# Optimization experiments

Measured on AMD Instinct MI355X. Metric: run time of the kernel, lower is better.

The kernel has to match this reference:

```python
import jax, jax.numpy as jnp
import numpy as np

N, D, H, K = 131072, 512, 128, 3
NPOS, NNEG = 8192, 8192
KM_ITERS = 4
PROTO_SHIFT = 0.15
PROTO_LOGIT_SCALE = 0.2
TEMP = 2.5


def _sq_cdist(x, c):
    # squared euclidean distance, matches torch.cdist(...).pow(2)
    d = jnp.sum(x * x, -1, keepdims=True) + jnp.sum(c * c, -1)[None, :] - 2.0 * (x @ c.T)
    return jnp.maximum(d, 0.0)


def _kmeans(x, k, iters):
    # torch.linspace(0, n-1, steps=k).long() init, fixed iteration count
    n = x.shape[0]
    idx = jnp.linspace(0.0, n - 1, k).astype(jnp.int32)
    centers = x[idx]
    for _ in range(iters):
        assign = jnp.argmin(_sq_cdist(x, centers), axis=1)
        sums = jax.ops.segment_sum(x, assign, num_segments=k)
        counts = jax.ops.segment_sum(jnp.ones((n,), x.dtype), assign, num_segments=k)[:, None]
        # empty cluster keeps old center (mask.any() branch in torch)
        centers = jnp.where(counts > 0, sums / jnp.maximum(counts, 1.0), centers)
    return centers


def setup_inputs() -> dict:
    key = jax.random.key(0)
    ks = jax.random.split(key, 10)
    s = 1.0 / np.sqrt(D).astype(np.float32)
    return {
        "z_cls": jax.random.normal(ks[0], (N, D), jnp.float32),
        "z_proto": jax.random.normal(ks[1], (N, D), jnp.float32),
        "pos_ctx": jax.random.normal(ks[2], (D,), jnp.float32),
        "neg_ctx": jax.random.normal(ks[3], (D,), jnp.float32),
        "W1": jax.random.normal(ks[4], (H, D), jnp.float32) * s,
        "b1": jnp.zeros((H,), jnp.float32),
        "W2": jax.random.normal(ks[5], (1, H), jnp.float32) * (1.0 / np.sqrt(H).astype(np.float32)),
        "b2": jnp.zeros((1,), jnp.float32),
        "Wp": jax.random.normal(ks[6], (D, D), jnp.float32) * s,
        "bp": jnp.zeros((D,), jnp.float32),
        "Wn": jax.random.normal(ks[7], (D, D), jnp.float32) * s,
        "bn": jnp.zeros((D,), jnp.float32),
        "pos_idx": jax.random.randint(ks[8], (NPOS,), 0, N),
        "neg_idx": jax.random.randint(ks[9], (NNEG,), 0, N),
    }


def reference(z_cls, z_proto, pos_ctx, neg_ctx, W1, b1, W2, b2, Wp, bp, Wn, bn, pos_idx, neg_idx):
    # _build_prototypes (pos_idx/neg_idx nonempty path)
    pos_proto = _kmeans(z_proto[pos_idx], K, KM_ITERS)          # [K, D]
    neg_proto = jnp.mean(z_proto[neg_idx], axis=0)              # [D]
    # _calibrate (ema not initialized -> no EMA blend)
    pos_proto = pos_proto + PROTO_SHIFT * (pos_ctx @ Wp.T + bp)[None, :]
    neg_proto = neg_proto + PROTO_SHIFT * (neg_ctx @ Wn.T + bn)
    # distances
    d_pos_all = _sq_cdist(z_proto, pos_proto)                   # [N, K]
    d_pos = jnp.min(d_pos_all, axis=1)
    pos_assign = jnp.argmin(d_pos_all, axis=1)
    d_neg = jnp.mean((z_proto - neg_proto[None, :]) ** 2, axis=1)
    proto_logit = (d_neg - d_pos) / np.sqrt(D).astype(np.float32)
    # cls head (eval mode: dropout is identity)
    h = jax.nn.relu(z_cls @ W1.T + b1)
    cls_logit = (h @ W2.T + b2)[:, 0]
    logits = (cls_logit + PROTO_LOGIT_SCALE * proto_logit) / TEMP
    prob = jax.nn.sigmoid(logits)
    return (logits, prob, PROTO_LOGIT_SCALE * proto_logit, pos_assign, d_pos_all, pos_proto, neg_proto)
```

## Files before the change

kernel.cpp:

```cpp
#include <hip/hip_runtime.h>
#include <hip/hip_bf16.h>

#define NPTS 131072
#define DIM  512
#define HID  128
#define KCL  3
#define NPOSI 8192
#define NNEGI 8192

typedef __attribute__((ext_vector_type(8))) short bf16x8;
typedef __attribute__((ext_vector_type(4))) float f32x4;

enum {
  WS_SHIFT_POS = 0,
  WS_SHIFT_NEG = 512,
  WS_NEGSUM    = 1024,
  WS_NEGPART   = 1536,
  WS_SUMS      = 67072,
  WS_W1BF      = 73228,
};
#define SUMS_STRIDE 1539

__device__ __forceinline__ short f2bf(float x) {
  __hip_bfloat16 h = __float2bfloat16(x);
  return *reinterpret_cast<short*>(&h);
}

__global__ __launch_bounds__(256) void k_prep(const float* __restrict__ W1,
                                              const float* __restrict__ Wp, const float* __restrict__ bp,
                                              const float* __restrict__ Wn, const float* __restrict__ bn,
                                              const float* __restrict__ pos_ctx, const float* __restrict__ neg_ctx,
                                              const float* __restrict__ zp, const int* __restrict__ neg_idx,
                                              float* __restrict__ ws) {
  int bid = blockIdx.x, t = threadIdx.x;
  if (bid < 256) {
    int i = bid * 256 + t;
    __hip_bfloat16* dst = (__hip_bfloat16*)(ws + WS_W1BF);
    dst[i] = __float2bfloat16(W1[i]);
  } else if (bid < 288) {
    int b = bid - 256;
    int mat = b >> 4;
    const float* W    = mat ? Wn : Wp;
    const float* bias = mat ? bn : bp;
    const float* ctx  = mat ? neg_ctx : pos_ctx;
    float* outp = ws + (mat ? WS_SHIFT_NEG : WS_SHIFT_POS);
    int row = (b & 15) * 32 + (t >> 3);
    int sub = t & 7;
    const float* wr = W + row * DIM + sub * 64;
    const float* cr = ctx + sub * 64;
    float s = 0.f;
#pragma unroll
    for (int j = 0; j < 64; j += 4) {
      float4 w4 = *(const float4*)(wr + j);
      float4 c4 = *(const float4*)(cr + j);
      s += w4.x * c4.x + w4.y * c4.y + w4.z * c4.z + w4.w * c4.w;
    }
    s += __shfl_xor(s, 1);
    s += __shfl_xor(s, 2);
    s += __shfl_xor(s, 4);
    if (sub == 0) outp[row] = 0.15f * (s + bias[row]);
  } else if (bid < 416) {
    int j = bid - 288;
    int c0 = t * 2;
    float a0 = 0.f, a1 = 0.f;
    int j0 = j * 64;
    for (int jj = 0; jj < 64; ++jj) {
      int row = neg_idx[j0 + jj];
      float2 v = *(const float2*)(zp + (size_t)row * DIM + c0);
      a0 += v.x; a1 += v.y;
    }
    ws[WS_NEGPART + j * DIM + c0]     = a0;
    ws[WS_NEGPART + j * DIM + c0 + 1] = a1;
  } else {
    for (int idx = t; idx < 4 * SUMS_STRIDE; idx += 256) ws[WS_SUMS + idx] = 0.f;
  }
}

template <int IT>
__global__ __launch_bounds__(256) void k_km(const float* __restrict__ zp,
                                            const int* __restrict__ pos_idx,
                                            float* __restrict__ ws) {
  int bid = blockIdx.x, t = threadIdx.x;
  if (IT == 0 && bid == 128) {
    int c0 = t * 2;
    float a0 = 0.f, a1 = 0.f;
#pragma unroll 8
    for (int j = 0; j < 128; ++j) {
      float2 v = *(const float2*)(ws + WS_NEGPART + j * DIM + c0);
      a0 += v.x; a1 += v.y;
    }
    ws[WS_NEGSUM + c0]     = a0;
    ws[WS_NEGSUM + c0 + 1] = a1;
    return;
  }
  __shared__ float cc[KCL * DIM];
  __shared__ float cn[KCL];
  __shared__ float lsum[KCL * DIM];
  __shared__ float lcnt[KCL];
  int w = t >> 6, l = t & 63;

  for (int idx = t; idx < KCL * DIM; idx += 256) lsum[idx] = 0.f;
  if (t < KCL) lcnt[t] = 0.f;

  for (int idx = t; idx < KCL * DIM; idx += 256) {
    int k = idx >> 9;
    int sel = (k == 0) ? 0 : ((k == 1) ? 4095 : 8191);
    float v = zp[(size_t)pos_idx[sel] * DIM + (idx & 511)];
#pragma unroll
    for (int j = 0; j < IT; ++j) {
      float cntv = ws[WS_SUMS + j * SUMS_STRIDE + 3 * DIM + k];
      float sv   = ws[WS_SUMS + j * SUMS_STRIDE + idx];
      v = (cntv > 0.f) ? sv / cntv : v;
    }
    cc[idx] = v;
  }
  __syncthreads();
  if (w < KCL) {
    float s = 0.f;
#pragma unroll
    for (int m = 0; m < 8; ++m) { float v = cc[w * DIM + l + m * 64]; s += v * v; }
#pragma unroll
    for (int m = 1; m < 64; m <<= 1) s += __shfl_xor(s, m);
    if (l == 0) cn[w] = s;
  }
  __syncthreads();

  float ck0[8], ck1[8], ck2[8];
#pragma unroll
  for (int j = 0; j < 8; ++j) {
    ck0[j] = cc[0 * DIM + l * 8 + j];
    ck1[j] = cc[1 * DIM + l * 8 + j];
    ck2[j] = cc[2 * DIM + l * 8 + j];
  }
  float cn0 = cn[0], cn1 = cn[1], cn2 = cn[2];
  float acc0[8] = {0,0,0,0,0,0,0,0}, acc1[8] = {0,0,0,0,0,0,0,0}, acc2[8] = {0,0,0,0,0,0,0,0};
  float cnt0 = 0.f, cnt1 = 0.f, cnt2 = 0.f;

  int wid = bid * 4 + w;
  for (int p = wid; p < NPOSI; p += 512) {
    int row = pos_idx[p];
    const float* xr = zp + (size_t)row * DIM + l * 8;
    float4 x0 = *(const float4*)(xr);
    float4 x1 = *(const float4*)(xr + 4);
    float x[8] = {x0.x, x0.y, x0.z, x0.w, x1.x, x1.y, x1.z, x1.w};
    float d0 = 0.f, d1 = 0.f, d2 = 0.f;
#pragma unroll
    for (int j = 0; j < 8; ++j) { d0 += x[j] * ck0[j]; d1 += x[j] * ck1[j]; d2 += x[j] * ck2[j]; }
#pragma unroll
    for (int m = 1; m < 64; m <<= 1) {
      d0 += __shfl_xor(d0, m); d1 += __shfl_xor(d1, m); d2 += __shfl_xor(d2, m);
    }
    float t0 = cn0 - 2.f * d0, t1 = cn1 - 2.f * d1, t2 = cn2 - 2.f * d2;
    int a = 0; float best = t0;
    if (t1 < best) { best = t1; a = 1; }
    if (t2 < best) { best = t2; a = 2; }
    if (a == 0)      { cnt0 += 1.f;
#pragma unroll
      for (int j = 0; j < 8; ++j) acc0[j] += x[j]; }
    else if (a == 1) { cnt1 += 1.f;
#pragma unroll
      for (int j = 0; j < 8; ++j) acc1[j] += x[j]; }
    else             { cnt2 += 1.f;
#pragma unroll
      for (int j = 0; j < 8; ++j) acc2[j] += x[j]; }
  }
#pragma unroll
  for (int j = 0; j < 8; ++j) {
    atomicAdd(&lsum[0 * DIM + l * 8 + j], acc0[j]);
    atomicAdd(&lsum[1 * DIM + l * 8 + j], acc1[j]);
    atomicAdd(&lsum[2 * DIM + l * 8 + j], acc2[j]);
  }
  if (l == 0) {
    atomicAdd(&lcnt[0], cnt0); atomicAdd(&lcnt[1], cnt1); atomicAdd(&lcnt[2], cnt2);
  }
  __syncthreads();
  for (int idx = t; idx < KCL * DIM; idx += 256) atomicAdd(&ws[WS_SUMS + IT * SUMS_STRIDE + idx], lsum[idx]);
  if (t < KCL) atomicAdd(&ws[WS_SUMS + IT * SUMS_STRIDE + 3 * DIM + t], lcnt[t]);
}

__global__ __launch_bounds__(256) void k_main(const float* __restrict__ zc,
                                              const float* __restrict__ zp,
                                              const float* __restrict__ b1,
                                              const float* __restrict__ W2,
                                              const float* __restrict__ b2,
                                              const int* __restrict__ pos_idx,
                                              const float* __restrict__ ws,
                                              float* __restrict__ out) {
  __shared__ float pp[KCL * DIM];
  __shared__ float np[DIM];
  __shared__ float pn[KCL + 1];
  __shared__ __hip_bfloat16 Bs[HID][40];
  __shared__ float clsv[64];
  __shared__ float outst[64 * 4 + 192];

  int t = threadIdx.x, w = t >> 6, l = t & 63;
  int i0 = blockIdx.x * 64;

  for (int idx = t; idx < KCL * DIM; idx += 256) {
    int k = idx >> 9, d = idx & 511;
    int sel = (k == 0) ? 0 : ((k == 1) ? 4095 : 8191);
    float v = zp[(size_t)pos_idx[sel] * DIM + d];
#pragma unroll
    for (int j = 0; j < 4; ++j) {
      float cntv = ws[WS_SUMS + j * SUMS_STRIDE + 3 * DIM + k];
      float sv   = ws[WS_SUMS + j * SUMS_STRIDE + idx];
      v = (cntv > 0.f) ? sv / cntv : v;
    }
    pp[idx] = v + ws[WS_SHIFT_POS + d];
  }
  for (int d = t; d < DIM; d += 256)
    np[d] = ws[WS_NEGSUM + d] * (1.f / NNEGI) + ws[WS_SHIFT_NEG + d];
  __syncthreads();
  {
    float s = 0.f;
    if (w < KCL) {
#pragma unroll
      for (int m = 0; m < 8; ++m) { float v = pp[w * DIM + l + m * 64]; s += v * v; }
    } else {
#pragma unroll
      for (int m = 0; m < 8; ++m) { float v = np[l + m * 64]; s += v * v; }
    }
#pragma unroll
    for (int m = 1; m < 64; m <<= 1) s += __shfl_xor(s, m);
    if (l == 0) pn[w] = s;
  }
  if (blockIdx.x == 0) {
    for (int idx = t; idx < KCL * DIM; idx += 256) out[7 * NPTS + idx] = pp[idx];
    for (int d = t; d < DIM; d += 256)            out[7 * NPTS + KCL * DIM + d] = np[d];
  }

  const __hip_bfloat16* W1bf = (const __hip_bfloat16*)(ws + WS_W1BF);
  f32x4 acc[8];
#pragma unroll
  for (int n = 0; n < 8; ++n) acc[n] = (f32x4){0.f, 0.f, 0.f, 0.f};
  int arow = i0 + w * 16 + (l & 15);
  const float* aptr = zc + (size_t)arow * DIM + (l >> 4) * 8;
  int srow = t >> 1, scol = (t & 1) * 16;

  for (int kc = 0; kc < DIM; kc += 32) {
    __syncthreads();
    {
      const float4* src = (const float4*)(W1bf + (size_t)srow * DIM + kc + scol);
      float4 v0 = src[0], v1 = src[1];
      *(float4*)(&Bs[srow][scol])     = v0;
      *(float4*)(&Bs[srow][scol + 8]) = v1;
    }
    __syncthreads();
    float4 a0 = *(const float4*)(aptr + kc);
    float4 a1 = *(const float4*)(aptr + kc + 4);
    bf16x8 af;
    af[0] = f2bf(a0.x); af[1] = f2bf(a0.y); af[2] = f2bf(a0.z); af[3] = f2bf(a0.w);
    af[4] = f2bf(a1.x); af[5] = f2bf(a1.y); af[6] = f2bf(a1.z); af[7] = f2bf(a1.w);
#pragma unroll
    for (int n = 0; n < 8; ++n) {
      bf16x8 bf = *(const bf16x8*)(&Bs[n * 16 + (l & 15)][(l >> 4) * 8]);
      acc[n] = __builtin_amdgcn_mfma_f32_16x16x32_bf16(af, bf, acc[n], 0, 0, 0);
    }
  }
  {
    float p[4] = {0.f, 0.f, 0.f, 0.f};
    int col_l = l & 15;
#pragma unroll
    for (int n = 0; n < 8; ++n) {
      int col = n * 16 + col_l;
      float bb = b1[col], w2 = W2[col];
#pragma unroll
      for (int r = 0; r < 4; ++r) {
        float h = acc[n][r] + bb;
        h = h > 0.f ? h : 0.f;
        p[r] += h * w2;
      }
    }
#pragma unroll
    for (int m = 1; m < 16; m <<= 1) {
#pragma unroll
      for (int r = 0; r < 4; ++r) p[r] += __shfl_xor(p[r], m);
    }
    if (col_l == 0) {
      float bias2 = b2[0];
      int rl = w * 16 + (l >> 4) * 4;
#pragma unroll
      for (int r = 0; r < 4; ++r) clsv[rl + r] = p[r] + bias2;
    }
  }
  __syncthreads();

  float ppr0[8], ppr1[8], ppr2[8], npr[8];
#pragma unroll
  for (int j = 0; j < 8; ++j) {
    ppr0[j] = pp[0 * DIM + l * 8 + j];
    ppr1[j] = pp[1 * DIM + l * 8 + j];
    ppr2[j] = pp[2 * DIM + l * 8 + j];
    npr[j]  = np[l * 8 + j];
  }
  float pn0 = pn[0], pn1 = pn[1], pn2 = pn[2], nn = pn[3];

  for (int r = 0; r < 16; ++r) {
    int rl = w * 16 + r;
    int i = i0 + rl;
    const float* xr = zp + (size_t)i * DIM + l * 8;
    float4 x0 = *(const float4*)(xr);
    float4 x1 = *(const float4*)(xr + 4);
    float x[8] = {x0.x, x0.y, x0.z, x0.w, x1.x, x1.y, x1.z, x1.w};
    float sx = 0.f, d0 = 0.f, d1 = 0.f, d2 = 0.f, dn = 0.f;
#pragma unroll
    for (int j = 0; j < 8; ++j) {
      sx += x[j] * x[j];
      d0 += x[j] * ppr0[j];
      d1 += x[j] * ppr1[j];
      d2 += x[j] * ppr2[j];
      dn += x[j] * npr[j];
    }
#pragma unroll
    for (int m = 1; m < 64; m <<= 1) {
      sx += __shfl_xor(sx, m);
      d0 += __shfl_xor(d0, m);
      d1 += __shfl_xor(d1, m);
      d2 += __shfl_xor(d2, m);
      dn += __shfl_xor(dn, m);
    }
    if (l == 0) {
      float e0 = sx + pn0 - 2.f * d0; e0 = e0 > 0.f ? e0 : 0.f;
      float e1 = sx + pn1 - 2.f * d1; e1 = e1 > 0.f ? e1 : 0.f;
      float e2 = sx + pn2 - 2.f * d2; e2 = e2 > 0.f ? e2 : 0.f;
      float dpos = e0; int a = 0;
      if (e1 < dpos) { dpos = e1; a = 1; }
      if (e2 < dpos) { dpos = e2; a = 2; }
      float dneg = (sx + nn - 2.f * dn) * (1.f / DIM);
      float plog = (dneg - dpos) * 0.04419417382415922f;
      float o2 = 0.2f * plog;
      float lg = (clsv[rl] + o2) * 0.4f;
      float prob = 1.f / (1.f + expf(-lg));
      outst[rl]       = lg;
      outst[64 + rl]  = prob;
      outst[128 + rl] = o2;
      outst[192 + rl] = (float)a;
      outst[256 + 3 * rl]     = e0;
      outst[256 + 3 * rl + 1] = e1;
      outst[256 + 3 * rl + 2] = e2;
    }
  }
  __syncthreads();
  if (t < 64) {
    out[i0 + t]            = outst[t];
    out[NPTS + i0 + t]     = outst[64 + t];
    out[2 * NPTS + i0 + t] = outst[128 + t];
    out[3 * NPTS + i0 + t] = outst[192 + t];
  } else {
    int u = t - 64;
    if (u < 192) out[4 * NPTS + 3 * i0 + u] = outst[256 + u];
  }
}

extern "C" void kernel_launch(void* const* d_in, const int* in_sizes, int n_in,
                              void* d_out, int out_size, void* d_ws, size_t ws_size,
                              hipStream_t stream) {
  const float* z_cls   = (const float*)d_in[0];
  const float* z_proto = (const float*)d_in[1];
  const float* pos_ctx = (const float*)d_in[2];
  const float* neg_ctx = (const float*)d_in[3];
  const float* W1      = (const float*)d_in[4];
  const float* b1      = (const float*)d_in[5];
  const float* W2      = (const float*)d_in[6];
  const float* b2      = (const float*)d_in[7];
  const float* Wp      = (const float*)d_in[8];
  const float* bp      = (const float*)d_in[9];
  const float* Wn      = (const float*)d_in[10];
  const float* bn      = (const float*)d_in[11];
  const int* pos_idx   = (const int*)d_in[12];
  const int* neg_idx   = (const int*)d_in[13];
  float* out           = (float*)d_out;
  float* ws            = (float*)d_ws;

  k_prep<<<417, 256, 0, stream>>>(W1, Wp, bp, Wn, bn, pos_ctx, neg_ctx, z_proto, neg_idx, ws);
  k_km<0><<<129, 256, 0, stream>>>(z_proto, pos_idx, ws);
  k_km<1><<<128, 256, 0, stream>>>(z_proto, pos_idx, ws);
  k_km<2><<<128, 256, 0, stream>>>(z_proto, pos_idx, ws);
  k_km<3><<<128, 256, 0, stream>>>(z_proto, pos_idx, ws);
  k_main<<<NPTS / 64, 256, 0, stream>>>(z_cls, z_proto, b1, W2, b2, pos_idx, ws, out);
}
```

Before: 294.6 us.

## Compute prototype distances with MFMA and pre-swizzle W1 into fragment layout

The main kernel now computes dot products against the three positive prototypes and the negative prototype with a bf16 MFMA, inside the same k-loop as the classifier GEMM. This replaces the per-row fp32 wave-reduction loop with its shuffle chains. W1 is converted once into MFMA fragment order in global memory, so the k-loop loads B fragments directly and no longer stages them through LDS with per-iteration barriers. The k-means kernels also run with twice as many blocks. The cost is bf16 precision for the distance dot products, which can flip argmin assignments and change d_pos values compared with fp32.

```diff
diff --git a/kernel.cpp b/kernel.cpp
--- a/kernel.cpp
+++ b/kernel.cpp
@@ -17,7 +17,7 @@
   WS_NEGSUM    = 1024,
   WS_NEGPART   = 1536,
   WS_SUMS      = 67072,
-  WS_W1BF      = 73228,
+  WS_W1FRAG    = 73232,
 };
 #define SUMS_STRIDE 1539
 
@@ -33,12 +33,22 @@
                                               const float* __restrict__ zp, const int* __restrict__ neg_idx,
                                               float* __restrict__ ws) {
   int bid = blockIdx.x, t = threadIdx.x;
-  if (bid < 256) {
-    int i = bid * 256 + t;
-    __hip_bfloat16* dst = (__hip_bfloat16*)(ws + WS_W1BF);
-    dst[i] = __float2bfloat16(W1[i]);
-  } else if (bid < 288) {
-    int b = bid - 256;
+  if (bid < 32) {
+    int fid = bid * 256 + t;
+    int kc = fid >> 9;
+    int n  = (fid >> 6) & 7;
+    int l  = fid & 63;
+    int row = n * 16 + (l & 15);
+    int col = kc * 32 + (l >> 4) * 8;
+    const float* src = W1 + (size_t)row * DIM + col;
+    float4 v0 = *(const float4*)(src);
+    float4 v1 = *(const float4*)(src + 4);
+    bf16x8 f;
+    f[0] = f2bf(v0.x); f[1] = f2bf(v0.y); f[2] = f2bf(v0.z); f[3] = f2bf(v0.w);
+    f[4] = f2bf(v1.x); f[5] = f2bf(v1.y); f[6] = f2bf(v1.z); f[7] = f2bf(v1.w);
+    ((bf16x8*)(ws + WS_W1FRAG))[fid] = f;
+  } else if (bid < 64) {
+    int b = bid - 32;
     int mat = b >> 4;
     const float* W    = mat ? Wn : Wp;
     const float* bias = mat ? bn : bp;
@@ -59,8 +69,8 @@
     s += __shfl_xor(s, 2);
     s += __shfl_xor(s, 4);
     if (sub == 0) outp[row] = 0.15f * (s + bias[row]);
-  } else if (bid < 416) {
-    int j = bid - 288;
+  } else if (bid < 192) {
+    int j = bid - 64;
     int c0 = t * 2;
     float a0 = 0.f, a1 = 0.f;
     int j0 = j * 64;
@@ -81,7 +91,7 @@
                                             const int* __restrict__ pos_idx,
                                             float* __restrict__ ws) {
   int bid = blockIdx.x, t = threadIdx.x;
-  if (IT == 0 && bid == 128) {
+  if (IT == 0 && bid == 256) {
     int c0 = t * 2;
     float a0 = 0.f, a1 = 0.f;
 #pragma unroll 8
@@ -137,7 +147,7 @@
   float cnt0 = 0.f, cnt1 = 0.f, cnt2 = 0.f;
 
   int wid = bid * 4 + w;
-  for (int p = wid; p < NPOSI; p += 512) {
+  for (int p = wid; p < NPOSI; p += 1024) {
     int row = pos_idx[p];
     const float* xr = zp + (size_t)row * DIM + l * 8;
     float4 x0 = *(const float4*)(xr);
@@ -188,10 +198,12 @@
                                               float* __restrict__ out) {
   __shared__ float pp[KCL * DIM];
   __shared__ float np[DIM];
-  __shared__ float pn[KCL + 1];
-  __shared__ __hip_bfloat16 Bs[HID][40];
+  __shared__ float pn[4];
   __shared__ float clsv[64];
-  __shared__ float outst[64 * 4 + 192];
+  __shared__ float sxs[64];
+  __shared__ float dstg[4][64];
+  __shared__ float outst[448];
+  __shared__ bf16x8 pfrag[1024];
 
   int t = threadIdx.x, w = t >> 6, l = t & 63;
   int i0 = blockIdx.x * 64;
@@ -213,132 +225,119 @@
   __syncthreads();
   {
     float s = 0.f;
-    if (w < KCL) {
-#pragma unroll
-      for (int m = 0; m < 8; ++m) { float v = pp[w * DIM + l + m * 64]; s += v * v; }
-    } else {
-#pragma unroll
-      for (int m = 0; m < 8; ++m) { float v = np[l + m * 64]; s += v * v; }
-    }
+    const float* src = (w < 3) ? (pp + w * DIM) : np;
+#pragma unroll
+    for (int m = 0; m < 8; ++m) { float v = src[l + m * 64]; s += v * v; }
 #pragma unroll
     for (int m = 1; m < 64; m <<= 1) s += __shfl_xor(s, m);
     if (l == 0) pn[w] = s;
+  }
+  for (int idx = t; idx < 1024; idx += 256) {
+    int kc = idx >> 6, ll = idx & 63, c = ll & 15, ko = (ll >> 4) * 8;
+    bf16x8 v;
+#pragma unroll
+    for (int j = 0; j < 8; ++j) {
+      float f = (c < 3) ? pp[c * DIM + kc * 32 + ko + j]
+                        : ((c == 3) ? np[kc * 32 + ko + j] : 0.f);
+      v[j] = f2bf(f);
+    }
+    pfrag[idx] = v;
   }
   if (blockIdx.x == 0) {
     for (int idx = t; idx < KCL * DIM; idx += 256) out[7 * NPTS + idx] = pp[idx];
     for (int d = t; d < DIM; d += 256)            out[7 * NPTS + KCL * DIM + d] = np[d];
   }
-
-  const __hip_bfloat16* W1bf = (const __hip_bfloat16*)(ws + WS_W1BF);
-  f32x4 acc[8];
-#pragma unroll
-  for (int n = 0; n < 8; ++n) acc[n] = (f32x4){0.f, 0.f, 0.f, 0.f};
+  __syncthreads();
+
+  const bf16x8* w1f = (const bf16x8*)(ws + WS_W1FRAG);
   int arow = i0 + w * 16 + (l & 15);
-  const float* aptr = zc + (size_t)arow * DIM + (l >> 4) * 8;
-  int srow = t >> 1, scol = (t & 1) * 16;
-
-  for (int kc = 0; kc < DIM; kc += 32) {
-    __syncthreads();
-    {
-      const float4* src = (const float4*)(W1bf + (size_t)srow * DIM + kc + scol);
-      float4 v0 = src[0], v1 = src[1];
-      *(float4*)(&Bs[srow][scol])     = v0;
-      *(float4*)(&Bs[srow][scol + 8]) = v1;
-    }
-    __syncthreads();
-    float4 a0 = *(const float4*)(aptr + kc);
-    float4 a1 = *(const float4*)(aptr + kc + 4);
-    bf16x8 af;
-    af[0] = f2bf(a0.x); af[1] = f2bf(a0.y); af[2] = f2bf(a0.z); af[3] = f2bf(a0.w);
-    af[4] = f2bf(a1.x); af[5] = f2bf(a1.y); af[6] = f2bf(a1.z); af[7] = f2bf(a1.w);
-#pragma unroll
-    for (int n = 0; n < 8; ++n) {
-      bf16x8 bf = *(const bf16x8*)(&Bs[n * 16 + (l & 15)][(l >> 4) * 8]);
-      acc[n] = __builtin_amdgcn_mfma_f32_16x16x32_bf16(af, bf, acc[n], 0, 0, 0);
-    }
-  }
+  const float* zcrow = zc + (size_t)arow * DIM + (l >> 4) * 8;
+  const float* zprow = zp + (size_t)arow * DIM + (l >> 4) * 8;
+
+  f32x4 accc[8];
+#pragma unroll
+  for (int n = 0; n < 8; ++n) accc[n] = (f32x4){0.f, 0.f, 0.f, 0.f};
+  f32x4 accd = (f32x4){0.f, 0.f, 0.f, 0.f};
+  float sx = 0.f;
+
+  for (int kc = 0; kc < 16; ++kc) {
+    float4 c0 = *(const float4*)(zcrow + kc * 32);
+    float4 c1 = *(const float4*)(zcrow + kc * 32 + 4);
+    float4 p0 = *(const float4*)(zprow + kc * 32);
+    float4 p1 = *(const float4*)(zprow + kc * 32 + 4);
+    bf16x8 af, ap;
+    af[0] = f2bf(c0.x); af[1] = f2bf(c0.y); af[2] = f2bf(c0.z); af[3] = f2bf(c0.w);
+    af[4] = f2bf(c1.x); af[5] = f2bf(c1.y); af[6] = f2bf(c1.z); af[7] = f2bf(c1.w);
+    ap[0] = f2bf(p0.x); ap[1] = f2bf(p0.y); ap[2] = f2bf(p0.z); ap[3] = f2bf(p0.w);
+    ap[4] = f2bf(p1.x); ap[5] = f2bf(p1.y); ap[6] = f2bf(p1.z); ap[7] = f2bf(p1.w);
+    sx += p0.x * p0.x + p0.y * p0.y + p0.z * p0.z + p0.w * p0.w
+        + p1.x * p1.x + p1.y * p1.y + p1.z * p1.z + p1.w * p1.w;
+    accd = __builtin_amdgcn_mfma_f32_16x16x32_bf16(ap, pfrag[kc * 64 + l], accd, 0, 0, 0);
+    const bf16x8* wrow = w1f + kc * 512 + l;
+#pragma unroll
+    for (int n = 0; n < 8; ++n)
+      accc[n] = __builtin_amdgcn_mfma_f32_16x16x32_bf16(af, wrow[n * 64], accc[n], 0, 0, 0);
+  }
+
+  sx += __shfl_xor(sx, 16);
+  sx += __shfl_xor(sx, 32);
+  if (l < 16) sxs[w * 16 + l] = sx;
+
   {
-    float p[4] = {0.f, 0.f, 0.f, 0.f};
+    float pcl[4] = {0.f, 0.f, 0.f, 0.f};
     int col_l = l & 15;
 #pragma unroll
     for (int n = 0; n < 8; ++n) {
       int col = n * 16 + col_l;
-      float bb = b1[col], w2 = W2[col];
+      float bb = b1[col], w2v = W2[col];
 #pragma unroll
       for (int r = 0; r < 4; ++r) {
-        float h = acc[n][r] + bb;
+        float h = accc[n][r] + bb;
         h = h > 0.f ? h : 0.f;
-        p[r] += h * w2;
+        pcl[r] += h * w2v;
       }
     }
 #pragma unroll
     for (int m = 1; m < 16; m <<= 1) {
 #pragma unroll
-      for (int r = 0; r < 4; ++r) p[r] += __shfl_xor(p[r], m);
+      for (int r = 0; r < 4; ++r) pcl[r] += __shfl_xor(pcl[r], m);
     }
     if (col_l == 0) {
-      float bias2 = b2[0];
-      int rl = w * 16 + (l >> 4) * 4;
-#pragma unroll
-      for (int r = 0; r < 4; ++r) clsv[rl + r] = p[r] + bias2;
-    }
-  }
-  __syncthreads();
-
-  float ppr0[8], ppr1[8], ppr2[8], npr[8];
-#pragma unroll
-  for (int j = 0; j < 8; ++j) {
-    ppr0[j] = pp[0 * DIM + l * 8 + j];
-    ppr1[j] = pp[1 * DIM + l * 8 + j];
-    ppr2[j] = pp[2 * DIM + l * 8 + j];
-    npr[j]  = np[l * 8 + j];
-  }
-  float pn0 = pn[0], pn1 = pn[1], pn2 = pn[2], nn = pn[3];
-
-  for (int r = 0; r < 16; ++r) {
-    int rl = w * 16 + r;
-    int i = i0 + rl;
-    const float* xr = zp + (size_t)i * DIM + l * 8;
-    float4 x0 = *(const float4*)(xr);
-    float4 x1 = *(const float4*)(xr + 4);
-    float x[8] = {x0.x, x0.y, x0.z, x0.w, x1.x, x1.y, x1.z, x1.w};
-    float sx = 0.f, d0 = 0.f, d1 = 0.f, d2 = 0.f, dn = 0.f;
-#pragma unroll
-    for (int j = 0; j < 8; ++j) {
-      sx += x[j] * x[j];
-      d0 += x[j] * ppr0[j];
-      d1 += x[j] * ppr1[j];
-      d2 += x[j] * ppr2[j];
-      dn += x[j] * npr[j];
-    }
-#pragma unroll
-    for (int m = 1; m < 64; m <<= 1) {
-      sx += __shfl_xor(sx, m);
-      d0 += __shfl_xor(d0, m);
-      d1 += __shfl_xor(d1, m);
-      d2 += __shfl_xor(d2, m);
-      dn += __shfl_xor(dn, m);
-    }
-    if (l == 0) {
-      float e0 = sx + pn0 - 2.f * d0; e0 = e0 > 0.f ? e0 : 0.f;
-      float e1 = sx + pn1 - 2.f * d1; e1 = e1 > 0.f ? e1 : 0.f;
-      float e2 = sx + pn2 - 2.f * d2; e2 = e2 > 0.f ? e2 : 0.f;
-      float dpos = e0; int a = 0;
-      if (e1 < dpos) { dpos = e1; a = 1; }
-      if (e2 < dpos) { dpos = e2; a = 2; }
-      float dneg = (sx + nn - 2.f * dn) * (1.f / DIM);
-      float plog = (dneg - dpos) * 0.04419417382415922f;
-      float o2 = 0.2f * plog;
-      float lg = (clsv[rl] + o2) * 0.4f;
-      float prob = 1.f / (1.f + expf(-lg));
-      outst[rl]       = lg;
-      outst[64 + rl]  = prob;
-      outst[128 + rl] = o2;
-      outst[192 + rl] = (float)a;
-      outst[256 + 3 * rl]     = e0;
-      outst[256 + 3 * rl + 1] = e1;
-      outst[256 + 3 * rl + 2] = e2;
-    }
+      float b2v = b2[0];
+#pragma unroll
+      for (int r = 0; r < 4; ++r) clsv[w * 16 + (l >> 4) * 4 + r] = pcl[r] + b2v;
+    }
+  }
+  {
+    int c = l & 15;
+    if (c < 4) {
+#pragma unroll
+      for (int j = 0; j < 4; ++j) dstg[c][w * 16 + (l >> 4) * 4 + j] = accd[j];
+    }
+  }
+  __syncthreads();
+
+  if (t < 64) {
+    float sxv = sxs[t];
+    float d0 = dstg[0][t], d1 = dstg[1][t], d2 = dstg[2][t], dn = dstg[3][t];
+    float e0 = sxv + pn[0] - 2.f * d0; e0 = fmaxf(e0, 0.f);
+    float e1 = sxv + pn[1] - 2.f * d1; e1 = fmaxf(e1, 0.f);
+    float e2 = sxv + pn[2] - 2.f * d2; e2 = fmaxf(e2, 0.f);
+    float dpos = e0; int a = 0;
+    if (e1 < dpos) { dpos = e1; a = 1; }
+    if (e2 < dpos) { dpos = e2; a = 2; }
+    float dneg = (sxv + pn[3] - 2.f * dn) * (1.f / DIM);
+    float plog = (dneg - dpos) * 0.04419417382415922f;
+    float o2 = 0.2f * plog;
+    float lg = (clsv[t] + o2) * 0.4f;
+    float prob = 1.f / (1.f + expf(-lg));
+    outst[t]        = lg;
+    outst[64 + t]   = prob;
+    outst[128 + t]  = o2;
+    outst[192 + t]  = (float)a;
+    outst[256 + 3 * t]     = e0;
+    outst[256 + 3 * t + 1] = e1;
+    outst[256 + 3 * t + 2] = e2;
   }
   __syncthreads();
   if (t < 64) {
@@ -372,10 +371,10 @@
   float* out           = (float*)d_out;
   float* ws            = (float*)d_ws;
 
-  k_prep<<<417, 256, 0, stream>>>(W1, Wp, bp, Wn, bn, pos_ctx, neg_ctx, z_proto, neg_idx, ws);
-  k_km<0><<<129, 256, 0, stream>>>(z_proto, pos_idx, ws);
-  k_km<1><<<128, 256, 0, stream>>>(z_proto, pos_idx, ws);
-  k_km<2><<<128, 256, 0, stream>>>(z_proto, pos_idx, ws);
-  k_km<3><<<128, 256, 0, stream>>>(z_proto, pos_idx, ws);
+  k_prep<<<193, 256, 0, stream>>>(W1, Wp, bp, Wn, bn, pos_ctx, neg_ctx, z_proto, neg_idx, ws);
+  k_km<0><<<257, 256, 0, stream>>>(z_proto, pos_idx, ws);
+  k_km<1><<<256, 256, 0, stream>>>(z_proto, pos_idx, ws);
+  k_km<2><<<256, 256, 0, stream>>>(z_proto, pos_idx, ws);
+  k_km<3><<<256, 256, 0, stream>>>(z_proto, pos_idx, ws);
   k_main<<<NPTS / 64, 256, 0, stream>>>(z_cls, z_proto, b1, W2, b2, pos_idx, ws, out);
 }
```

Measured after the change: 289.9 us. Within noise of the previous version (-1.6%).
